# Kernel optimization log

Hardware: AMD Instinct MI355X
Metric: run time of the kernel (lower is better)

The kernel has to match this reference:

```python
import jax, jax.numpy as jnp
import numpy as np

EMBED_DIM = 1024
NUM_HEADS = 16
HEAD_DIM = EMBED_DIM // NUM_HEADS
SCALE = HEAD_DIM ** -0.5


def setup_inputs() -> dict:
    key = jax.random.key(0)
    ks = jax.random.split(key, 12)
    B, S, D = 4, 2048, EMBED_DIM
    s = 0.02
    return {
        "query": jax.random.normal(ks[0], (B, S, D), jnp.float32),
        "key": jax.random.normal(ks[1], (B, S, D), jnp.float32),
        "value": jax.random.normal(ks[2], (B, S, D), jnp.float32),
        "Wq": jax.random.normal(ks[3], (D, D), jnp.float32) * s,
        "bq": jnp.zeros((D,), jnp.float32),
        "Wk": jax.random.normal(ks[4], (D, D), jnp.float32) * s,
        "bk": jnp.zeros((D,), jnp.float32),
        "Wv": jax.random.normal(ks[5], (D, D), jnp.float32) * s,
        "bv": jnp.zeros((D,), jnp.float32),
        "Wo": jax.random.normal(ks[6], (D, D), jnp.float32) * s,
        "bo": jnp.zeros((D,), jnp.float32),
    }


def reference(query, key, value, Wq, bq, Wk, bk, Wv, bv, Wo, bo):
    B, S, D = query.shape
    H, Hd = NUM_HEADS, HEAD_DIM

    # Linear projections (torch Linear: x @ W^T + b)
    q = query @ Wq.T + bq
    k = key @ Wk.T + bk
    v = value @ Wv.T + bv

    # [B, H, S, Hd]
    q = q.reshape(B, S, H, Hd).transpose(0, 2, 1, 3)
    k = k.reshape(B, -1, H, Hd).transpose(0, 2, 1, 3)
    v = v.reshape(B, -1, H, Hd).transpose(0, 2, 1, 3)

    # scores: [B, H, S, Skv]
    scores = jnp.einsum("bhsd,bhtd->bhst", q, k) * SCALE

    # is_causal=True: mask strictly upper triangle
    Skv = k.shape[2]
    causal = jnp.triu(jnp.ones((S, Skv), dtype=bool), k=1)
    scores = jnp.where(causal, -jnp.inf, scores)

    attn = jax.nn.softmax(scores, axis=-1)
    out = jnp.einsum("bhst,bhtd->bhsd", attn, v)  # [B, H, S, Hd]
    out = out.transpose(0, 2, 1, 3).reshape(B, S, D)
    output = out @ Wo.T + bo

    # need_weights=True, average_attn_weights=True -> mean over heads
    attn_weights = attn.mean(axis=1)  # [B, S, Skv]
    return output, attn_weights
```

## Files before the change

kernel.cpp:

```cpp
#include <hip/hip_runtime.h>
#include <hip/hip_bf16.h>
#include <cmath>
#include <type_traits>

#define BC     4
#define SEQ    2048
#define DMODEL 1024
#define NHEAD  16
#define HD     64
#define ASCALE 0.125f
#define LOG2E  1.44269504f

typedef __bf16 bf16x8 __attribute__((ext_vector_type(8)));
typedef __bf16 bf16x4 __attribute__((ext_vector_type(4)));
typedef float  f32x4  __attribute__((ext_vector_type(4)));

__device__ __forceinline__ f32x4 mfma16x16x32(bf16x8 a, bf16x8 b, f32x4 c) {
    return __builtin_amdgcn_mfma_f32_16x16x32_bf16(a, b, c, 0, 0, 0);
}

__device__ __forceinline__ float fexp2(float x) {
    return __builtin_amdgcn_exp2f(x);
}

__device__ __forceinline__ void gload_lds16(const __bf16* g, __bf16* l) {
    __builtin_amdgcn_global_load_lds(
        (const __attribute__((address_space(1))) void*)g,
        (__attribute__((address_space(3))) void*)l, 16, 0, 0);
}

__global__ __launch_bounds__(256) void cvt_w(const float* __restrict__ a,
                                             const float* __restrict__ b,
                                             const float* __restrict__ c,
                                             const float* __restrict__ d,
                                             __bf16* __restrict__ oa,
                                             __bf16* __restrict__ ob,
                                             __bf16* __restrict__ oc,
                                             __bf16* __restrict__ od) {
    const float* in; __bf16* out;
    if (blockIdx.y == 0)      { in = a; out = oa; }
    else if (blockIdx.y == 1) { in = b; out = ob; }
    else if (blockIdx.y == 2) { in = c; out = oc; }
    else                      { in = d; out = od; }
    const size_t i = ((size_t)blockIdx.x * 256 + threadIdx.x) * 8;
    float4 f0 = *(const float4*)(in + i);
    float4 f1 = *(const float4*)(in + i + 4);
    bf16x8 o;
    o[0] = (__bf16)f0.x; o[1] = (__bf16)f0.y; o[2] = (__bf16)f0.z; o[3] = (__bf16)f0.w;
    o[4] = (__bf16)f1.x; o[5] = (__bf16)f1.y; o[6] = (__bf16)f1.z; o[7] = (__bf16)f1.w;
    *(bf16x8*)(out + i) = o;
}

__global__ __launch_bounds__(256) void qkv_gemm(const float* __restrict__ Aq,
                                                const float* __restrict__ Ak,
                                                const float* __restrict__ Av,
                                                const __bf16* __restrict__ Wqb,
                                                const __bf16* __restrict__ Wkb,
                                                const __bf16* __restrict__ Wvb,
                                                const float* __restrict__ bq,
                                                const float* __restrict__ bk,
                                                const float* __restrict__ bv,
                                                __bf16* __restrict__ oq,
                                                __bf16* __restrict__ ok,
                                                __bf16* __restrict__ ov) {
    constexpr int K = DMODEL, N = DMODEL;
    __shared__ __bf16 As[128 * 64];
    __shared__ __bf16 Bs[128 * 64];
    const int z = blockIdx.z;
    const float* A; const __bf16* W; const float* bias; __bf16* out; float scale; bool vt;
    if (z == 0)      { A = Aq; W = Wqb; bias = bq; out = oq; scale = ASCALE * LOG2E; vt = false; }
    else if (z == 1) { A = Ak; W = Wkb; bias = bk; out = ok; scale = 1.f; vt = false; }
    else             { A = Av; W = Wvb; bias = bv; out = ov; scale = 1.f; vt = true; }

    const int tid = threadIdx.x;
    const int lane = tid & 63;
    const int wid = tid >> 6;
    const int lr = lane & 15;
    const int lg = lane >> 4;
    const int wr = (wid >> 1) * 64;
    const int wc = (wid & 1) * 64;
    const int bm = blockIdx.x * 128;
    const int bn = blockIdx.y * 128;

    f32x4 acc[4][4] = {};

    float4 a0[4], a1[4];
    #pragma unroll
    for (int i = 0; i < 4; ++i) {
        const int p = tid + 256 * i;
        const int row = p >> 3, c = p & 7;
        const float* ap = A + (size_t)(bm + row) * K + c * 8;
        a0[i] = ((const float4*)ap)[0];
        a1[i] = ((const float4*)ap)[1];
    }

    for (int k0 = 0; k0 < K; k0 += 64) {
        #pragma unroll
        for (int i = 0; i < 4; ++i) {
            const int p = tid + 256 * i;
            const int row = p >> 3, c = p & 7;
            const int csrc = ((c ^ (row & 7)) * 8);
            gload_lds16(W + (size_t)(bn + row) * K + k0 + csrc, &Bs[p * 8]);
        }
        #pragma unroll
        for (int i = 0; i < 4; ++i) {
            const int p = tid + 256 * i;
            const int row = p >> 3, c = p & 7;
            bf16x8 v;
            v[0] = (__bf16)a0[i].x; v[1] = (__bf16)a0[i].y;
            v[2] = (__bf16)a0[i].z; v[3] = (__bf16)a0[i].w;
            v[4] = (__bf16)a1[i].x; v[5] = (__bf16)a1[i].y;
            v[6] = (__bf16)a1[i].z; v[7] = (__bf16)a1[i].w;
            *(bf16x8*)&As[row * 64 + ((c ^ (row & 7)) * 8)] = v;
        }
        __syncthreads();

        if (k0 + 64 < K) {
            #pragma unroll
            for (int i = 0; i < 4; ++i) {
                const int p = tid + 256 * i;
                const int row = p >> 3, c = p & 7;
                const float* ap = A + (size_t)(bm + row) * K + k0 + 64 + c * 8;
                a0[i] = ((const float4*)ap)[0];
                a1[i] = ((const float4*)ap)[1];
            }
        }

        #pragma unroll
        for (int kk = 0; kk < 2; ++kk) {
            bf16x8 af[4], bfg[4];
            #pragma unroll
            for (int m = 0; m < 4; ++m) {
                const int row = wr + m * 16 + lr;
                af[m] = *(const bf16x8*)&As[row * 64 + ((kk * 4 + lg) ^ (row & 7)) * 8];
            }
            #pragma unroll
            for (int n = 0; n < 4; ++n) {
                const int row = wc + n * 16 + lr;
                bfg[n] = *(const bf16x8*)&Bs[row * 64 + ((kk * 4 + lg) ^ (row & 7)) * 8];
            }
            #pragma unroll
            for (int m = 0; m < 4; ++m)
                #pragma unroll
                for (int n = 0; n < 4; ++n)
                    acc[m][n] = mfma16x16x32(af[m], bfg[n], acc[m][n]);
        }
        __syncthreads();
    }

    #pragma unroll
    for (int n = 0; n < 4; ++n) {
        const int col = bn + wc + n * 16 + lr;
        const float bb = bias[col];
        #pragma unroll
        for (int m = 0; m < 4; ++m) {
            const int row0 = bm + wr + m * 16 + lg * 4;
            if (vt) {
                const int h = col >> 6, hd = col & 63;
                const int b = row0 >> 11, s = row0 & 2047;
                bf16x4 pk;
                #pragma unroll
                for (int r = 0; r < 4; ++r) pk[r] = (__bf16)((acc[m][n][r] + bb) * scale);
                *(bf16x4*)(out + (((size_t)b * NHEAD + h) * HD + hd) * SEQ + s) = pk;
            } else {
                #pragma unroll
                for (int r = 0; r < 4; ++r)
                    out[(size_t)(row0 + r) * N + col] = (__bf16)((acc[m][n][r] + bb) * scale);
            }
        }
    }
}

__global__ __launch_bounds__(256) void gemm_out(const __bf16* __restrict__ A,
                                                const __bf16* __restrict__ W,
                                                const float* __restrict__ bias,
                                                float* __restrict__ out) {
    constexpr int K = DMODEL, N = DMODEL;
    __shared__ __bf16 As[128 * 64];
    __shared__ __bf16 Bs[128 * 64];
    const int tid = threadIdx.x;
    const int lane = tid & 63;
    const int wid = tid >> 6;
    const int lr = lane & 15;
    const int lg = lane >> 4;
    const int wr = (wid >> 1) * 64;
    const int wc = (wid & 1) * 64;
    const int bm = blockIdx.x * 128;
    const int bn = blockIdx.y * 128;

    f32x4 acc[4][4] = {};

    for (int k0 = 0; k0 < K; k0 += 64) {
        #pragma unroll
        for (int i = 0; i < 4; ++i) {
            const int p = tid + 256 * i;
            const int row = p >> 3, c = p & 7;
            const int csrc = ((c ^ (row & 7)) * 8);
            gload_lds16(W + (size_t)(bn + row) * K + k0 + csrc, &Bs[p * 8]);
            gload_lds16(A + (size_t)(bm + row) * K + k0 + csrc, &As[p * 8]);
        }
        __syncthreads();

        #pragma unroll
        for (int kk = 0; kk < 2; ++kk) {
            bf16x8 af[4], bfg[4];
            #pragma unroll
            for (int m = 0; m < 4; ++m) {
                const int row = wr + m * 16 + lr;
                af[m] = *(const bf16x8*)&As[row * 64 + ((kk * 4 + lg) ^ (row & 7)) * 8];
            }
            #pragma unroll
            for (int n = 0; n < 4; ++n) {
                const int row = wc + n * 16 + lr;
                bfg[n] = *(const bf16x8*)&Bs[row * 64 + ((kk * 4 + lg) ^ (row & 7)) * 8];
            }
            #pragma unroll
            for (int m = 0; m < 4; ++m)
                #pragma unroll
                for (int n = 0; n < 4; ++n)
                    acc[m][n] = mfma16x16x32(af[m], bfg[n], acc[m][n]);
        }
        __syncthreads();
    }

    #pragma unroll
    for (int n = 0; n < 4; ++n) {
        const int col = bn + wc + n * 16 + lr;
        const float bb = bias[col];
        #pragma unroll
        for (int m = 0; m < 4; ++m) {
            const int row0 = bm + wr + m * 16 + lg * 4;
            #pragma unroll
            for (int r = 0; r < 4; ++r)
                out[(size_t)(row0 + r) * N + col] = acc[m][n][r] + bb;
        }
    }
}

__global__ __launch_bounds__(512) void flash_fwd(const __bf16* __restrict__ q,
                                                 const __bf16* __restrict__ k,
                                                 const __bf16* __restrict__ vt,
                                                 __bf16* __restrict__ o,
                                                 float* __restrict__ mbuf,
                                                 float* __restrict__ lbuf) {
    __shared__ __bf16 Ks[2][64][64];
    __shared__ __bf16 Vs[2][64][64];
    __shared__ __bf16 Ps[8][16][64];
    const int tid = threadIdx.x;
    const int lane = tid & 63;
    const int wid = tid >> 6;
    const int lr = lane & 15;
    const int lg = lane >> 4;

    const int flat = blockIdx.x;
    const int xcd = flat & 7;
    const int slot = flat >> 3;
    const int group = xcd * 8 + (slot >> 4);
    const int b = group >> 4;
    const int h = group & 15;
    const int qt = 15 - (slot & 15);

    const int qr = qt * 128 + wid * 16;
    const int myq = qr + lr;
    const int dtile = qr >> 6;

    bf16x8 qf0, qf1;
    {
        const __bf16* qp = q + (size_t)(b * SEQ + myq) * DMODEL + h * HD + lg * 8;
        qf0 = ((const bf16x8*)qp)[0];
        qf1 = *(const bf16x8*)(qp + 32);
    }

    float m_run = -INFINITY;
    float l_run = 0.f;
    f32x4 oacc[4] = {};

    const int srow = tid >> 3;
    const int sc = tid & 7;
    const int swz = (sc ^ (srow & 7)) * 8;
    const int rsw = (lr & 7);
    const int nt = 2 * qt + 2;

    const __bf16* kbase = k + (size_t)(b * SEQ + srow) * DMODEL + h * HD + sc * 8;
    const __bf16* vbase = vt + ((size_t)(b * NHEAD + h) * HD + srow) * SEQ + sc * 8;

    {
        bf16x8 kr = *(const bf16x8*)kbase;
        bf16x8 vr = *(const bf16x8*)vbase;
        *(bf16x8*)&Ks[0][srow][swz] = kr;
        *(bf16x8*)&Vs[0][srow][swz] = vr;
    }
    __syncthreads();

    for (int t = 0; t < nt; ++t) {
        const int buf = t & 1;
        const bool pre = (t + 1 < nt);
        bf16x8 kr, vr;
        if (pre) {
            kr = *(const bf16x8*)(kbase + (size_t)(t + 1) * 64 * DMODEL);
            vr = *(const bf16x8*)(vbase + (t + 1) * 64);
        }

        if (t <= dtile) {
            f32x4 z[4];
            __builtin_amdgcn_s_setprio(1);
            #pragma unroll
            for (int ts = 0; ts < 4; ++ts) {
                bf16x8 kf0 = *(const bf16x8*)&Ks[buf][ts * 16 + lr][(lg ^ rsw) * 8];
                bf16x8 kf1 = *(const bf16x8*)&Ks[buf][ts * 16 + lr][((4 + lg) ^ rsw) * 8];
                f32x4 acc = {0.f, 0.f, 0.f, 0.f};
                acc = mfma16x16x32(kf0, qf0, acc);
                acc = mfma16x16x32(kf1, qf1, acc);
                z[ts] = acc;
            }
            __builtin_amdgcn_s_setprio(0);

            if (t == dtile) {
                #pragma unroll
                for (int ts = 0; ts < 4; ++ts)
                    #pragma unroll
                    for (int r = 0; r < 4; ++r)
                        if (t * 64 + ts * 16 + lg * 4 + r > myq) z[ts][r] = -INFINITY;
            }

            float a0 = fmaxf(fmaxf(z[0][0], z[0][1]), z[0][2]);
            float a1 = fmaxf(fmaxf(z[0][3], z[1][0]), z[1][1]);
            float a2 = fmaxf(fmaxf(z[1][2], z[1][3]), z[2][0]);
            float a3 = fmaxf(fmaxf(z[2][1], z[2][2]), z[2][3]);
            float a4 = fmaxf(fmaxf(z[3][0], z[3][1]), z[3][2]);
            float a5 = z[3][3];
            float b0 = fmaxf(fmaxf(a0, a1), a2);
            float b1 = fmaxf(fmaxf(a3, a4), a5);
            const float mt = fmaxf(b0, b1);

            if (!__all(mt <= m_run + 11.54f)) {
                float mr = fmaxf(mt, __shfl_xor(mt, 16));
                mr = fmaxf(mr, __shfl_xor(mr, 32));
                const float mnew = fmaxf(m_run, mr);
                const float alpha = fexp2(m_run - mnew);
                #pragma unroll
                for (int r = 0; r < 4; ++r) {
                    const float ar = __shfl(alpha, lg * 4 + r);
                    #pragma unroll
                    for (int hf = 0; hf < 4; ++hf) oacc[hf][r] *= ar;
                }
                l_run *= alpha;
                m_run = mnew;
            }

            float rsum = 0.f;
            #pragma unroll
            for (int ts = 0; ts < 4; ++ts) {
                bf16x4 pk;
                #pragma unroll
                for (int r = 0; r < 4; ++r) {
                    float pv = fexp2(z[ts][r] - m_run);
                    rsum += pv;
                    pk[r] = (__bf16)pv;
                }
                *(bf16x4*)&Ps[wid][lr][((ts * 2 + (lg >> 1)) ^ rsw) * 8 + (lg & 1) * 4] = pk;
            }
            l_run += rsum;

            bf16x8 pf0 = *(const bf16x8*)&Ps[wid][lr][(lg ^ rsw) * 8];
            bf16x8 pf1 = *(const bf16x8*)&Ps[wid][lr][((4 + lg) ^ rsw) * 8];
            __builtin_amdgcn_s_setprio(1);
            #pragma unroll
            for (int hf = 0; hf < 4; ++hf) {
                bf16x8 vf0 = *(const bf16x8*)&Vs[buf][hf * 16 + lr][(lg ^ rsw) * 8];
                bf16x8 vf1 = *(const bf16x8*)&Vs[buf][hf * 16 + lr][((4 + lg) ^ rsw) * 8];
                oacc[hf] = mfma16x16x32(pf0, vf0, oacc[hf]);
                oacc[hf] = mfma16x16x32(pf1, vf1, oacc[hf]);
            }
            __builtin_amdgcn_s_setprio(0);
        }

        if (pre) {
            *(bf16x8*)&Ks[buf ^ 1][srow][swz] = kr;
            *(bf16x8*)&Vs[buf ^ 1][srow][swz] = vr;
        }
        __syncthreads();
    }

    l_run += __shfl_xor(l_run, 16);
    l_run += __shfl_xor(l_run, 32);

    const float linv = 1.f / l_run;
    #pragma unroll
    for (int r = 0; r < 4; ++r) {
        const float li = __shfl(linv, lg * 4 + r);
        #pragma unroll
        for (int hf = 0; hf < 4; ++hf)
            o[(size_t)(b * SEQ + qr + lg * 4 + r) * DMODEL + h * HD + hf * 16 + lr] =
                (__bf16)(oacc[hf][r] * li);
    }
    if (lg == 0) {
        mbuf[((size_t)b * SEQ + myq) * NHEAD + h] = m_run;
        lbuf[((size_t)b * SEQ + myq) * NHEAD + h] = l_run;
    }
}

__global__ __launch_bounds__(512) void attn_weights(const __bf16* __restrict__ q,
                                                    const __bf16* __restrict__ k,
                                                    const float* __restrict__ mbuf,
                                                    const float* __restrict__ lbuf,
                                                    float* __restrict__ wout) {
    __shared__ __bf16 Ks[2][128][64];
    const int flat = blockIdx.x;
    const int xcd = flat & 7;
    const int slot = flat >> 3;
    const int gi = slot >> 4;
    const int st = slot & 15;
    const int b = gi & 3;
    const int t2 = (gi >> 2) ? (15 - xcd) : xcd;

    const int tid = threadIdx.x;
    const int lane = tid & 63;
    const int wid = tid >> 6;
    const int lr = lane & 15;
    const int lg = lane >> 4;
    const int myq = st * 128 + wid * 16 + lr;
    const int k0 = t2 * 128;

    float* wp = wout + (size_t)(b * SEQ + myq) * SEQ + k0 + lg * 4;

    if (t2 > st) {
        const f32x4 zz = {0.f, 0.f, 0.f, 0.f};
        #pragma unroll
        for (int ts = 0; ts < 8; ++ts) *(f32x4*)(wp + ts * 16) = zz;
        return;
    }
    const bool needmask = (t2 == st);

    f32x4 rm[4], rl[4];
    {
        const float* mp = mbuf + ((size_t)b * SEQ + myq) * NHEAD;
        const float* lp = lbuf + ((size_t)b * SEQ + myq) * NHEAD;
        #pragma unroll
        for (int i = 0; i < 4; ++i) rm[i] = *(const f32x4*)(mp + i * 4);
        #pragma unroll
        for (int i = 0; i < 4; ++i) {
            f32x4 t = *(const f32x4*)(lp + i * 4);
            #pragma unroll
            for (int r = 0; r < 4; ++r) rl[i][r] = 1.f / (t[r] * (float)NHEAD);
        }
    }

    const int srow = tid >> 2;
    const int scb = (tid & 3) * 2;
    const int rsw = (lr & 7);
    const __bf16* krow = k + (size_t)(b * SEQ + k0 + srow) * DMODEL + scb * 8;
    const __bf16* qbase = q + (size_t)(b * SEQ + myq) * DMODEL + lg * 8;

    {
        bf16x8 kr[2];
        #pragma unroll
        for (int c = 0; c < 2; ++c) kr[c] = *(const bf16x8*)(krow + c * 8);
        #pragma unroll
        for (int c = 0; c < 2; ++c)
            *(bf16x8*)&Ks[0][srow][((scb + c) ^ (srow & 7)) * 8] = kr[c];
    }
    bf16x8 qna = ((const bf16x8*)qbase)[0];
    bf16x8 qnb = *(const bf16x8*)(qbase + 32);

    f32x4 wacc[8] = {};
    __syncthreads();

    #pragma unroll
    for (int h = 0; h < NHEAD; ++h) {
        const int cur = h & 1;
        bf16x8 kr[2];
        if (h + 1 < NHEAD) {
            const __bf16* kp = krow + (h + 1) * HD;
            #pragma unroll
            for (int c = 0; c < 2; ++c) kr[c] = *(const bf16x8*)(kp + c * 8);
        }
        const bf16x8 qf0 = qna, qf1 = qnb;
        if (h + 1 < NHEAD) {
            qna = *(const bf16x8*)(qbase + (h + 1) * HD);
            qnb = *(const bf16x8*)(qbase + (h + 1) * HD + 32);
        }
        const float rmh = rm[h >> 2][h & 3];
        const float rlh = rl[h >> 2][h & 3];

        #pragma unroll
        for (int ts = 0; ts < 8; ++ts) {
            bf16x8 kf0 = *(const bf16x8*)&Ks[cur][ts * 16 + lr][(lg ^ rsw) * 8];
            bf16x8 kf1 = *(const bf16x8*)&Ks[cur][ts * 16 + lr][((4 + lg) ^ rsw) * 8];
            f32x4 zz = {0.f, 0.f, 0.f, 0.f};
            zz = mfma16x16x32(kf0, qf0, zz);
            zz = mfma16x16x32(kf1, qf1, zz);
            if (needmask) {
                #pragma unroll
                for (int r = 0; r < 4; ++r) {
                    float e = 0.f;
                    if (k0 + ts * 16 + lg * 4 + r <= myq)
                        e = fexp2(zz[r] - rmh) * rlh;
                    wacc[ts][r] += e;
                }
            } else {
                #pragma unroll
                for (int r = 0; r < 4; ++r)
                    wacc[ts][r] += fexp2(zz[r] - rmh) * rlh;
            }
        }

        if (h + 1 < NHEAD) {
            #pragma unroll
            for (int c = 0; c < 2; ++c)
                *(bf16x8*)&Ks[cur ^ 1][srow][((scb + c) ^ (srow & 7)) * 8] = kr[c];
        }
        __syncthreads();
    }

    #pragma unroll
    for (int ts = 0; ts < 8; ++ts)
        *(f32x4*)(wp + ts * 16) = wacc[ts];
}

extern "C" void kernel_launch(void* const* d_in, const int* in_sizes, int n_in,
                              void* d_out, int out_size, void* d_ws, size_t ws_size,
                              hipStream_t stream) {
    const float* query = (const float*)d_in[0];
    const float* key_  = (const float*)d_in[1];
    const float* value = (const float*)d_in[2];
    const float* Wq = (const float*)d_in[3];
    const float* bq = (const float*)d_in[4];
    const float* Wk = (const float*)d_in[5];
    const float* bk = (const float*)d_in[6];
    const float* Wv = (const float*)d_in[7];
    const float* bv = (const float*)d_in[8];
    const float* Wo = (const float*)d_in[9];
    const float* bo = (const float*)d_in[10];
    float* out = (float*)d_out;

    const size_t nelem = (size_t)BC * SEQ * DMODEL;
    char* p = (char*)d_ws;
    const size_t mat = nelem * sizeof(__bf16);
    __bf16* qb  = (__bf16*)p; p += mat;
    __bf16* kb  = (__bf16*)p; p += mat;
    __bf16* vtb = (__bf16*)p; p += mat;
    __bf16* ob  = (__bf16*)p; p += mat;
    const size_t wmat = (size_t)DMODEL * DMODEL * sizeof(__bf16);
    __bf16* wqb = (__bf16*)p; p += wmat;
    __bf16* wkb = (__bf16*)p; p += wmat;
    __bf16* wvb = (__bf16*)p; p += wmat;
    __bf16* wob = (__bf16*)p; p += wmat;
    float* mb = (float*)p; p += (size_t)BC * NHEAD * SEQ * sizeof(float);
    float* lb = (float*)p; p += (size_t)BC * NHEAD * SEQ * sizeof(float);

    float* wout = out + nelem;

    cvt_w<<<dim3(DMODEL * DMODEL / 2048, 4), 256, 0, stream>>>(Wq, Wk, Wv, Wo, wqb, wkb, wvb, wob);

    const int M = BC * SEQ;
    qkv_gemm<<<dim3(M / 128, DMODEL / 128, 3), 256, 0, stream>>>(
        query, key_, value, wqb, wkb, wvb, bq, bk, bv, qb, kb, vtb);

    flash_fwd<<<dim3(1024), 512, 0, stream>>>(qb, kb, vtb, ob, mb, lb);
    gemm_out<<<dim3(M / 128, DMODEL / 128), 256, 0, stream>>>(ob, wob, bo, out);

    attn_weights<<<dim3(1024), 512, 0, stream>>>(qb, kb, mb, lb, wout);
}
```

Baseline: 272.4 us.

## Double-buffer weight tiles in QKV GEMM to overlap global loads with MFMA

The QKV projection GEMM now keeps two LDS buffers for the weight tile and issues the next tile's direct-to-LDS weight loads and register-staged activation loads before computing on the current tile. Weight fetch latency can then overlap the MFMA work, where before it sat between barriers on the critical path. The cost is double the weight LDS footprint, which may reduce occupancy, and an extra barrier per iteration after writing the converted activations to LDS.

```diff
diff --git a/kernel.cpp b/kernel.cpp
--- a/kernel.cpp
+++ b/kernel.cpp
@@ -63,9 +63,9 @@
                                                 __bf16* __restrict__ oq,
                                                 __bf16* __restrict__ ok,
                                                 __bf16* __restrict__ ov) {
-    constexpr int K = DMODEL, N = DMODEL;
+    constexpr int K = DMODEL, N = DMODEL, NT = K / 64;
     __shared__ __bf16 As[128 * 64];
-    __shared__ __bf16 Bs[128 * 64];
+    __shared__ __bf16 Bs[2][128 * 64];
     const int z = blockIdx.z;
     const float* A; const __bf16* W; const float* bias; __bf16* out; float scale; bool vt;
     if (z == 0)      { A = Aq; W = Wqb; bias = bq; out = oq; scale = ASCALE * LOG2E; vt = false; }
@@ -85,22 +85,21 @@
     f32x4 acc[4][4] = {};
 
     float4 a0[4], a1[4];
-    #pragma unroll
-    for (int i = 0; i < 4; ++i) {
-        const int p = tid + 256 * i;
-        const int row = p >> 3, c = p & 7;
-        const float* ap = A + (size_t)(bm + row) * K + c * 8;
-        a0[i] = ((const float4*)ap)[0];
-        a1[i] = ((const float4*)ap)[1];
-    }
-
-    for (int k0 = 0; k0 < K; k0 += 64) {
+    {
+        #pragma unroll
+        for (int i = 0; i < 4; ++i) {
+            const int p = tid + 256 * i;
+            const int row = p >> 3, c = p & 7;
+            const float* ap = A + (size_t)(bm + row) * K + c * 8;
+            a0[i] = ((const float4*)ap)[0];
+            a1[i] = ((const float4*)ap)[1];
+        }
         #pragma unroll
         for (int i = 0; i < 4; ++i) {
             const int p = tid + 256 * i;
             const int row = p >> 3, c = p & 7;
             const int csrc = ((c ^ (row & 7)) * 8);
-            gload_lds16(W + (size_t)(bn + row) * K + k0 + csrc, &Bs[p * 8]);
+            gload_lds16(W + (size_t)(bn + row) * K + csrc, &Bs[0][p * 8]);
         }
         #pragma unroll
         for (int i = 0; i < 4; ++i) {
@@ -114,13 +113,25 @@
             *(bf16x8*)&As[row * 64 + ((c ^ (row & 7)) * 8)] = v;
         }
         __syncthreads();
-
-        if (k0 + 64 < K) {
+    }
+
+    for (int t = 0; t < NT; ++t) {
+        const int buf = t & 1;
+        const bool pre = (t + 1 < NT);
+        if (pre) {
+            const int k1 = (t + 1) * 64;
             #pragma unroll
             for (int i = 0; i < 4; ++i) {
                 const int p = tid + 256 * i;
                 const int row = p >> 3, c = p & 7;
-                const float* ap = A + (size_t)(bm + row) * K + k0 + 64 + c * 8;
+                const int csrc = ((c ^ (row & 7)) * 8);
+                gload_lds16(W + (size_t)(bn + row) * K + k1 + csrc, &Bs[buf ^ 1][p * 8]);
+            }
+            #pragma unroll
+            for (int i = 0; i < 4; ++i) {
+                const int p = tid + 256 * i;
+                const int row = p >> 3, c = p & 7;
+                const float* ap = A + (size_t)(bm + row) * K + k1 + c * 8;
                 a0[i] = ((const float4*)ap)[0];
                 a1[i] = ((const float4*)ap)[1];
             }
@@ -137,7 +148,7 @@
             #pragma unroll
             for (int n = 0; n < 4; ++n) {
                 const int row = wc + n * 16 + lr;
-                bfg[n] = *(const bf16x8*)&Bs[row * 64 + ((kk * 4 + lg) ^ (row & 7)) * 8];
+                bfg[n] = *(const bf16x8*)&Bs[buf][row * 64 + ((kk * 4 + lg) ^ (row & 7)) * 8];
             }
             #pragma unroll
             for (int m = 0; m < 4; ++m)
@@ -146,6 +157,21 @@
                     acc[m][n] = mfma16x16x32(af[m], bfg[n], acc[m][n]);
         }
         __syncthreads();
+
+        if (pre) {
+            #pragma unroll
+            for (int i = 0; i < 4; ++i) {
+                const int p = tid + 256 * i;
+                const int row = p >> 3, c = p & 7;
+                bf16x8 v;
+                v[0] = (__bf16)a0[i].x; v[1] = (__bf16)a0[i].y;
+                v[2] = (__bf16)a0[i].z; v[3] = (__bf16)a0[i].w;
+                v[4] = (__bf16)a1[i].x; v[5] = (__bf16)a1[i].y;
+                v[6] = (__bf16)a1[i].z; v[7] = (__bf16)a1[i].w;
+                *(bf16x8*)&As[row * 64 + ((c ^ (row & 7)) * 8)] = v;
+            }
+            __syncthreads();
+        }
     }
 
     #pragma unroll
```

New measurement: 299.0 us. 9.8% more time.

## Fuse output projection GEMM and attention-weights kernel into one launch

Applied to the files above, without the earlier changes.

Merges the output-projection GEMM and the attention-weight averaging kernel into a single launch, with the first 512 blocks doing the GEMM and the remaining 1024 computing attention weights. To fit the shared 512-thread block, the GEMM warp tiling changes from 4 warps of 64x64 to 8 warps of 64x32. The two independent tails can now run concurrently on the GPU, filling idle CUs and saving one launch. The cost is a larger combined kernel, whose register and shared-memory footprint is set by the heavier branch and may lower occupancy.

```diff
diff --git a/kernel.cpp b/kernel.cpp
--- a/kernel.cpp
+++ b/kernel.cpp
@@ -171,69 +171,188 @@
     }
 }
 
-__global__ __launch_bounds__(256) void gemm_out(const __bf16* __restrict__ A,
-                                                const __bf16* __restrict__ W,
-                                                const float* __restrict__ bias,
-                                                float* __restrict__ out) {
-    constexpr int K = DMODEL, N = DMODEL;
-    __shared__ __bf16 As[128 * 64];
-    __shared__ __bf16 Bs[128 * 64];
+__global__ __launch_bounds__(512) void tail_fused(const __bf16* __restrict__ ob,
+                                                  const __bf16* __restrict__ Wob,
+                                                  const float* __restrict__ bo,
+                                                  float* __restrict__ out,
+                                                  const __bf16* __restrict__ q,
+                                                  const __bf16* __restrict__ k,
+                                                  const float* __restrict__ mbuf,
+                                                  const float* __restrict__ lbuf,
+                                                  float* __restrict__ wout) {
+    __shared__ __bf16 smem[2][128][64];
     const int tid = threadIdx.x;
     const int lane = tid & 63;
     const int wid = tid >> 6;
     const int lr = lane & 15;
     const int lg = lane >> 4;
-    const int wr = (wid >> 1) * 64;
-    const int wc = (wid & 1) * 64;
-    const int bm = blockIdx.x * 128;
-    const int bn = blockIdx.y * 128;
-
-    f32x4 acc[4][4] = {};
-
-    for (int k0 = 0; k0 < K; k0 += 64) {
-        #pragma unroll
-        for (int i = 0; i < 4; ++i) {
-            const int p = tid + 256 * i;
-            const int row = p >> 3, c = p & 7;
-            const int csrc = ((c ^ (row & 7)) * 8);
-            gload_lds16(W + (size_t)(bn + row) * K + k0 + csrc, &Bs[p * 8]);
-            gload_lds16(A + (size_t)(bm + row) * K + k0 + csrc, &As[p * 8]);
-        }
+
+    if (blockIdx.x < 512) {
+        constexpr int K = DMODEL, N = DMODEL;
+        __bf16* As = &smem[0][0][0];
+        __bf16* Bs = &smem[1][0][0];
+        const int bx = blockIdx.x;
+        const int bm = (bx & 63) * 128;
+        const int bn = (bx >> 6) * 128;
+        const int wr = (wid >> 2) * 64;
+        const int wc = (wid & 3) * 32;
+
+        f32x4 acc[4][2] = {};
+
+        for (int k0 = 0; k0 < K; k0 += 64) {
+            #pragma unroll
+            for (int i = 0; i < 2; ++i) {
+                const int p = tid + 512 * i;
+                const int row = p >> 3, c = p & 7;
+                const int csrc = ((c ^ (row & 7)) * 8);
+                gload_lds16(Wob + (size_t)(bn + row) * K + k0 + csrc, &Bs[p * 8]);
+                gload_lds16(ob  + (size_t)(bm + row) * K + k0 + csrc, &As[p * 8]);
+            }
+            __syncthreads();
+
+            #pragma unroll
+            for (int kk = 0; kk < 2; ++kk) {
+                bf16x8 af[4], bfg[2];
+                #pragma unroll
+                for (int m = 0; m < 4; ++m) {
+                    const int row = wr + m * 16 + lr;
+                    af[m] = *(const bf16x8*)&As[row * 64 + ((kk * 4 + lg) ^ (row & 7)) * 8];
+                }
+                #pragma unroll
+                for (int n = 0; n < 2; ++n) {
+                    const int row = wc + n * 16 + lr;
+                    bfg[n] = *(const bf16x8*)&Bs[row * 64 + ((kk * 4 + lg) ^ (row & 7)) * 8];
+                }
+                #pragma unroll
+                for (int m = 0; m < 4; ++m)
+                    #pragma unroll
+                    for (int n = 0; n < 2; ++n)
+                        acc[m][n] = mfma16x16x32(af[m], bfg[n], acc[m][n]);
+            }
+            __syncthreads();
+        }
+
+        #pragma unroll
+        for (int n = 0; n < 2; ++n) {
+            const int col = bn + wc + n * 16 + lr;
+            const float bb = bo[col];
+            #pragma unroll
+            for (int m = 0; m < 4; ++m) {
+                const int row0 = bm + wr + m * 16 + lg * 4;
+                #pragma unroll
+                for (int r = 0; r < 4; ++r)
+                    out[(size_t)(row0 + r) * N + col] = acc[m][n][r] + bb;
+            }
+        }
+        return;
+    }
+
+    {
+        const int flat = blockIdx.x - 512;
+        const int xcd = flat & 7;
+        const int slot = flat >> 3;
+        const int gi = slot >> 4;
+        const int st = slot & 15;
+        const int b = gi & 3;
+        const int t2 = (gi >> 2) ? (15 - xcd) : xcd;
+
+        const int myq = st * 128 + wid * 16 + lr;
+        const int k0 = t2 * 128;
+
+        float* wp = wout + (size_t)(b * SEQ + myq) * SEQ + k0 + lg * 4;
+
+        if (t2 > st) {
+            const f32x4 zz = {0.f, 0.f, 0.f, 0.f};
+            #pragma unroll
+            for (int ts = 0; ts < 8; ++ts) *(f32x4*)(wp + ts * 16) = zz;
+            return;
+        }
+        const bool needmask = (t2 == st);
+
+        f32x4 rm[4], rl[4];
+        {
+            const float* mp = mbuf + ((size_t)b * SEQ + myq) * NHEAD;
+            const float* lp = lbuf + ((size_t)b * SEQ + myq) * NHEAD;
+            #pragma unroll
+            for (int i = 0; i < 4; ++i) rm[i] = *(const f32x4*)(mp + i * 4);
+            #pragma unroll
+            for (int i = 0; i < 4; ++i) {
+                f32x4 t = *(const f32x4*)(lp + i * 4);
+                #pragma unroll
+                for (int r = 0; r < 4; ++r) rl[i][r] = 1.f / (t[r] * (float)NHEAD);
+            }
+        }
+
+        const int srow = tid >> 2;
+        const int scb = (tid & 3) * 2;
+        const int rsw = (lr & 7);
+        const __bf16* krow = k + (size_t)(b * SEQ + k0 + srow) * DMODEL + scb * 8;
+        const __bf16* qbase = q + (size_t)(b * SEQ + myq) * DMODEL + lg * 8;
+
+        {
+            bf16x8 kr[2];
+            #pragma unroll
+            for (int c = 0; c < 2; ++c) kr[c] = *(const bf16x8*)(krow + c * 8);
+            #pragma unroll
+            for (int c = 0; c < 2; ++c)
+                *(bf16x8*)&smem[0][srow][((scb + c) ^ (srow & 7)) * 8] = kr[c];
+        }
+        bf16x8 qna = ((const bf16x8*)qbase)[0];
+        bf16x8 qnb = *(const bf16x8*)(qbase + 32);
+
+        f32x4 wacc[8] = {};
         __syncthreads();
 
         #pragma unroll
-        for (int kk = 0; kk < 2; ++kk) {
-            bf16x8 af[4], bfg[4];
-            #pragma unroll
-            for (int m = 0; m < 4; ++m) {
-                const int row = wr + m * 16 + lr;
-                af[m] = *(const bf16x8*)&As[row * 64 + ((kk * 4 + lg) ^ (row & 7)) * 8];
-            }
-            #pragma unroll
-            for (int n = 0; n < 4; ++n) {
-                const int row = wc + n * 16 + lr;
-                bfg[n] = *(const bf16x8*)&Bs[row * 64 + ((kk * 4 + lg) ^ (row & 7)) * 8];
-            }
-            #pragma unroll
-            for (int m = 0; m < 4; ++m)
-                #pragma unroll
-                for (int n = 0; n < 4; ++n)
-                    acc[m][n] = mfma16x16x32(af[m], bfg[n], acc[m][n]);
-        }
-        __syncthreads();
-    }
-
-    #pragma unroll
-    for (int n = 0; n < 4; ++n) {
-        const int col = bn + wc + n * 16 + lr;
-        const float bb = bias[col];
-        #pragma unroll
-        for (int m = 0; m < 4; ++m) {
-            const int row0 = bm + wr + m * 16 + lg * 4;
-            #pragma unroll
-            for (int r = 0; r < 4; ++r)
-                out[(size_t)(row0 + r) * N + col] = acc[m][n][r] + bb;
-        }
+        for (int h = 0; h < NHEAD; ++h) {
+            const int cur = h & 1;
+            bf16x8 kr[2];
+            if (h + 1 < NHEAD) {
+                const __bf16* kp = krow + (h + 1) * HD;
+                #pragma unroll
+                for (int c = 0; c < 2; ++c) kr[c] = *(const bf16x8*)(kp + c * 8);
+            }
+            const bf16x8 qf0 = qna, qf1 = qnb;
+            if (h + 1 < NHEAD) {
+                qna = *(const bf16x8*)(qbase + (h + 1) * HD);
+                qnb = *(const bf16x8*)(qbase + (h + 1) * HD + 32);
+            }
+            const float rmh = rm[h >> 2][h & 3];
+            const float rlh = rl[h >> 2][h & 3];
+
+            #pragma unroll
+            for (int ts = 0; ts < 8; ++ts) {
+                bf16x8 kf0 = *(const bf16x8*)&smem[cur][ts * 16 + lr][(lg ^ rsw) * 8];
+                bf16x8 kf1 = *(const bf16x8*)&smem[cur][ts * 16 + lr][((4 + lg) ^ rsw) * 8];
+                f32x4 zz = {0.f, 0.f, 0.f, 0.f};
+                zz = mfma16x16x32(kf0, qf0, zz);
+                zz = mfma16x16x32(kf1, qf1, zz);
+                if (needmask) {
+                    #pragma unroll
+                    for (int r = 0; r < 4; ++r) {
+                        float e = 0.f;
+                        if (k0 + ts * 16 + lg * 4 + r <= myq)
+                            e = fexp2(zz[r] - rmh) * rlh;
+                        wacc[ts][r] += e;
+                    }
+                } else {
+                    #pragma unroll
+                    for (int r = 0; r < 4; ++r)
+                        wacc[ts][r] += fexp2(zz[r] - rmh) * rlh;
+                }
+            }
+
+            if (h + 1 < NHEAD) {
+                #pragma unroll
+                for (int c = 0; c < 2; ++c)
+                    *(bf16x8*)&smem[cur ^ 1][srow][((scb + c) ^ (srow & 7)) * 8] = kr[c];
+            }
+            __syncthreads();
+        }
+
+        #pragma unroll
+        for (int ts = 0; ts < 8; ++ts)
+            *(f32x4*)(wp + ts * 16) = wacc[ts];
     }
 }
 
@@ -398,124 +517,6 @@
         mbuf[((size_t)b * SEQ + myq) * NHEAD + h] = m_run;
         lbuf[((size_t)b * SEQ + myq) * NHEAD + h] = l_run;
     }
-}
-
-__global__ __launch_bounds__(512) void attn_weights(const __bf16* __restrict__ q,
-                                                    const __bf16* __restrict__ k,
-                                                    const float* __restrict__ mbuf,
-                                                    const float* __restrict__ lbuf,
-                                                    float* __restrict__ wout) {
-    __shared__ __bf16 Ks[2][128][64];
-    const int flat = blockIdx.x;
-    const int xcd = flat & 7;
-    const int slot = flat >> 3;
-    const int gi = slot >> 4;
-    const int st = slot & 15;
-    const int b = gi & 3;
-    const int t2 = (gi >> 2) ? (15 - xcd) : xcd;
-
-    const int tid = threadIdx.x;
-    const int lane = tid & 63;
-    const int wid = tid >> 6;
-    const int lr = lane & 15;
-    const int lg = lane >> 4;
-    const int myq = st * 128 + wid * 16 + lr;
-    const int k0 = t2 * 128;
-
-    float* wp = wout + (size_t)(b * SEQ + myq) * SEQ + k0 + lg * 4;
-
-    if (t2 > st) {
-        const f32x4 zz = {0.f, 0.f, 0.f, 0.f};
-        #pragma unroll
-        for (int ts = 0; ts < 8; ++ts) *(f32x4*)(wp + ts * 16) = zz;
-        return;
-    }
-    const bool needmask = (t2 == st);
-
-    f32x4 rm[4], rl[4];
-    {
-        const float* mp = mbuf + ((size_t)b * SEQ + myq) * NHEAD;
-        const float* lp = lbuf + ((size_t)b * SEQ + myq) * NHEAD;
-        #pragma unroll
-        for (int i = 0; i < 4; ++i) rm[i] = *(const f32x4*)(mp + i * 4);
-        #pragma unroll
-        for (int i = 0; i < 4; ++i) {
-            f32x4 t = *(const f32x4*)(lp + i * 4);
-            #pragma unroll
-            for (int r = 0; r < 4; ++r) rl[i][r] = 1.f / (t[r] * (float)NHEAD);
-        }
-    }
-
-    const int srow = tid >> 2;
-    const int scb = (tid & 3) * 2;
-    const int rsw = (lr & 7);
-    const __bf16* krow = k + (size_t)(b * SEQ + k0 + srow) * DMODEL + scb * 8;
-    const __bf16* qbase = q + (size_t)(b * SEQ + myq) * DMODEL + lg * 8;
-
-    {
-        bf16x8 kr[2];
-        #pragma unroll
-        for (int c = 0; c < 2; ++c) kr[c] = *(const bf16x8*)(krow + c * 8);
-        #pragma unroll
-        for (int c = 0; c < 2; ++c)
-            *(bf16x8*)&Ks[0][srow][((scb + c) ^ (srow & 7)) * 8] = kr[c];
-    }
-    bf16x8 qna = ((const bf16x8*)qbase)[0];
-    bf16x8 qnb = *(const bf16x8*)(qbase + 32);
-
-    f32x4 wacc[8] = {};
-    __syncthreads();
-
-    #pragma unroll
-    for (int h = 0; h < NHEAD; ++h) {
-        const int cur = h & 1;
-        bf16x8 kr[2];
-        if (h + 1 < NHEAD) {
-            const __bf16* kp = krow + (h + 1) * HD;
-            #pragma unroll
-            for (int c = 0; c < 2; ++c) kr[c] = *(const bf16x8*)(kp + c * 8);
-        }
-        const bf16x8 qf0 = qna, qf1 = qnb;
-        if (h + 1 < NHEAD) {
-            qna = *(const bf16x8*)(qbase + (h + 1) * HD);
-            qnb = *(const bf16x8*)(qbase + (h + 1) * HD + 32);
-        }
-        const float rmh = rm[h >> 2][h & 3];
-        const float rlh = rl[h >> 2][h & 3];
-
-        #pragma unroll
-        for (int ts = 0; ts < 8; ++ts) {
-            bf16x8 kf0 = *(const bf16x8*)&Ks[cur][ts * 16 + lr][(lg ^ rsw) * 8];
-            bf16x8 kf1 = *(const bf16x8*)&Ks[cur][ts * 16 + lr][((4 + lg) ^ rsw) * 8];
-            f32x4 zz = {0.f, 0.f, 0.f, 0.f};
-            zz = mfma16x16x32(kf0, qf0, zz);
-            zz = mfma16x16x32(kf1, qf1, zz);
-            if (needmask) {
-                #pragma unroll
-                for (int r = 0; r < 4; ++r) {
-                    float e = 0.f;
-                    if (k0 + ts * 16 + lg * 4 + r <= myq)
-                        e = fexp2(zz[r] - rmh) * rlh;
-                    wacc[ts][r] += e;
-                }
-            } else {
-                #pragma unroll
-                for (int r = 0; r < 4; ++r)
-                    wacc[ts][r] += fexp2(zz[r] - rmh) * rlh;
-            }
-        }
-
-        if (h + 1 < NHEAD) {
-            #pragma unroll
-            for (int c = 0; c < 2; ++c)
-                *(bf16x8*)&Ks[cur ^ 1][srow][((scb + c) ^ (srow & 7)) * 8] = kr[c];
-        }
-        __syncthreads();
-    }
-
-    #pragma unroll
-    for (int ts = 0; ts < 8; ++ts)
-        *(f32x4*)(wp + ts * 16) = wacc[ts];
 }
 
 extern "C" void kernel_launch(void* const* d_in, const int* in_sizes, int n_in,
@@ -558,7 +559,6 @@
         query, key_, value, wqb, wkb, wvb, bq, bk, bv, qb, kb, vtb);
 
     flash_fwd<<<dim3(1024), 512, 0, stream>>>(qb, kb, vtb, ob, mb, lb);
-    gemm_out<<<dim3(M / 128, DMODEL / 128), 256, 0, stream>>>(ob, wob, bo, out);
-
-    attn_weights<<<dim3(1024), 512, 0, stream>>>(qb, kb, mb, lb, wout);
-}
+
+    tail_fused<<<dim3(1536), 512, 0, stream>>>(ob, wob, bo, out, qb, kb, mb, lb, wout);
+}
```

New measurement: 264.6 us. 1.03x faster.
